# Kernel tuning notes

Measured on AMD Instinct MI355X. Metric: run time of the kernel, lower is better.

Reference implementation:

```python
import jax, jax.numpy as jnp
import numpy as np

B, S, R, C_Q, C_KV, H, C_A = 1, 128, 256, 256, 256, 8, 32


def setup_inputs() -> dict:
    key = jax.random.key(0)
    ks = jax.random.split(key, 11)
    scale = 0.02
    q = jax.random.normal(ks[0], (B, S, R, C_Q), jnp.float32)
    kv = jax.random.normal(ks[1], (B, S, R, C_KV), jnp.float32)
    bias = jax.random.normal(ks[2], (B, 1, R, R, H), jnp.float32)
    bias_mask = jax.random.randint(ks[3], (B, S, R), 0, 2).astype(jnp.float32)
    w_q = jax.random.normal(ks[4], (C_Q, H, C_A), jnp.float32) * scale
    w_k = jax.random.normal(ks[5], (C_KV, H, C_A), jnp.float32) * scale
    w_v = jax.random.normal(ks[6], (C_KV, H, C_A), jnp.float32) * scale
    w_g = jax.random.normal(ks[7], (C_Q, H, C_A), jnp.float32) * scale
    b_g = jax.random.normal(ks[8], (H, C_A), jnp.float32) * scale
    w_o = jax.random.normal(ks[9], (H, C_A, C_Q), jnp.float32) * scale
    b_o = jax.random.normal(ks[10], (C_Q,), jnp.float32) * scale
    return {"q": q, "kv": kv, "bias": bias, "bias_mask": bias_mask,
            "w_q": w_q, "w_k": w_k, "w_v": w_v, "w_g": w_g, "b_g": b_g,
            "w_o": w_o, "b_o": b_o}


def reference(q, kv, bias, bias_mask, w_q, w_k, w_v, w_g, b_g, w_o, b_o):
    # q, kv: [B, S, R, C]; attention over residue dim R within each row s.
    c_a = w_q.shape[-1]
    normsize = 1.0 / jnp.sqrt(jnp.asarray(c_a, q.dtype))
    Q = jnp.einsum('bsqc,chd->bsqhd', q, w_q) * normsize  # [B,S,R,H,Ca]
    K = jnp.einsum('bskc,chd->bskhd', kv, w_k)
    V = jnp.einsum('bskc,chd->bskhd', kv, w_v)
    # affinity: [B,S,Q,K,H]
    AT = jnp.einsum('bsqhd,bskhd->bsqkh', Q, K)
    mask_bias = (bias_mask[:, :, None, :, None] - 1.0) * 1e9  # [B,S,1,K,1]
    AT = AT + bias + mask_bias
    AT = jax.nn.softmax(AT, axis=-2)  # softmax over K
    O = jnp.einsum('bsqkh,bskhd->bsqhd', AT, V)
    G = jax.nn.sigmoid(jnp.einsum('bsqc,chd->bsqhd', q, w_g) + b_g)
    O = O * G
    out = jnp.einsum('bsqhd,hdc->bsqc', O, w_o) + b_o  # [B,S,R,C_Q]
    return out
```

## Files before the change

kernel.cpp:

```cpp
#include <hip/hip_runtime.h>

typedef __bf16 bf16;
typedef __bf16 bf16x8 __attribute__((ext_vector_type(8)));
typedef float  f32x4  __attribute__((ext_vector_type(4)));
typedef unsigned int u32;

#define MFMA16(a, b, c) __builtin_amdgcn_mfma_f32_16x16x32_bf16((a), (b), (c), 0, 0, 0)


typedef __attribute__((address_space(3))) u32 lds_u32;
typedef const __attribute__((address_space(1))) u32 glob_u32;
__device__ __forceinline__ void gll16(const void* g, void* l) {
    __builtin_amdgcn_global_load_lds((glob_u32*)g, (lds_u32*)l, 16, 0, 0);
}

__global__ __launch_bounds__(256) void prep_kernel(
    const float* __restrict__ q, const float* __restrict__ kv,
    const float* __restrict__ bias,
    const float* __restrict__ w_q, const float* __restrict__ w_k,
    const float* __restrict__ w_v, const float* __restrict__ w_g,
    const float* __restrict__ w_o,
    bf16* __restrict__ qbf, bf16* __restrict__ kvbf, float* __restrict__ biasT,
    bf16* __restrict__ Wqg, bf16* __restrict__ Wkv, bf16* __restrict__ Wo)
{
    const float norm = 0.17677669529663687f;
    const int gid = blockIdx.x * 256 + threadIdx.x;
    const int gsz = gridDim.x * 256;

    for (int u = gid; u < 2097152; u += gsz) {
        const float* src; bf16* dst;
        if (u < 1048576) { src = q + (size_t)u * 8;            dst = qbf  + (size_t)u * 8; }
        else             { src = kv + (size_t)(u - 1048576)*8; dst = kvbf + (size_t)(u - 1048576)*8; }
        float4 x0 = *(const float4*)(src);
        float4 x1 = *(const float4*)(src + 4);
        bf16x8 t;
        t[0]=(bf16)x0.x; t[1]=(bf16)x0.y; t[2]=(bf16)x0.z; t[3]=(bf16)x0.w;
        t[4]=(bf16)x1.x; t[5]=(bf16)x1.y; t[6]=(bf16)x1.z; t[7]=(bf16)x1.w;
        *(bf16x8*)dst = t;
    }
    for (int u = gid; u < 524288; u += gsz) {
        int h = u >> 16, qq = (u >> 8) & 255, kk = u & 255;
        biasT[u] = bias[(((qq << 8) + kk) << 3) + h];
    }
    for (int u = gid; u < 131072; u += gsz) {
        int n = u >> 8, k = u & 255;
        float v = (n < 256) ? w_q[k * 256 + n] * norm : w_g[k * 256 + (n - 256)];
        Wqg[u] = (bf16)v;
    }
    for (int u = gid; u < 131072; u += gsz) {
        int n = u >> 8, k = u & 255;
        float v = (n < 256) ? w_k[k * 256 + n] : w_v[k * 256 + (n - 256)];
        Wkv[u] = (bf16)v;
    }
    for (int u = gid; u < 65536; u += gsz) {
        int n = u >> 8, k = u & 255;
        Wo[u] = (bf16)w_o[k * 256 + n];
    }
}

template<bool F32OUT>
__device__ __forceinline__ void gemm_core(
    const bf16* __restrict__ A, const bf16* __restrict__ Bw,
    bf16* __restrict__ Cb, float* __restrict__ Cf, const float* __restrict__ bo,
    int m0, int n0, int ntot)
{
    __shared__ __align__(16) bf16 As[128 * 32];
    __shared__ __align__(16) bf16 Bs[128 * 32];

    const int tid  = threadIdx.x;
    const int lane = tid & 63, wave = tid >> 6;
    const int quad = lane >> 4, lc = lane & 15;
    const int wr = wave >> 1, wc = wave & 1;

    const int r0 = tid >> 2, p0 = tid & 3;
    const int c1 = tid + 256;
    const int r1 = (c1 & 255) >> 2, p1 = c1 & 3;
    const bf16* gA0 = A  + (size_t)(m0 + r0) * 256 + p0 * 8;
    const bf16* gA1 = A  + (size_t)(m0 + 64 + r0) * 256 + p0 * 8;
    const bf16* gB0 = Bw + (size_t)(n0 + r0) * 256 + p0 * 8;
    const bf16* gB1 = Bw + (size_t)(n0 + 64 + r0) * 256 + p0 * 8;
    bf16* lA0 = As + tid * 8;
    bf16* lA1 = As + (tid + 256) * 8;
    bf16* lB0 = Bs + tid * 8;
    bf16* lB1 = Bs + (tid + 256) * 8;
    (void)r1; (void)p1;

    f32x4 acc[4][4];
    #pragma unroll
    for (int i = 0; i < 4; ++i)
        #pragma unroll
        for (int j = 0; j < 4; ++j) acc[i][j] = f32x4{0.f, 0.f, 0.f, 0.f};

    #pragma unroll 1
    for (int kb = 0; kb < 8; ++kb) {
        const int ko = kb * 32;
        gll16(gA0 + ko, lA0);
        gll16(gA1 + ko, lA1);
        gll16(gB0 + ko, lB0);
        gll16(gB1 + ko, lB1);
        __syncthreads();

        bf16x8 aF[4], bF[4];
        #pragma unroll
        for (int mt = 0; mt < 4; ++mt)
            aF[mt] = *(const bf16x8*)(As + (wr * 64 + mt * 16 + lc) * 32 + quad * 8);
        #pragma unroll
        for (int nt = 0; nt < 4; ++nt)
            bF[nt] = *(const bf16x8*)(Bs + (wc * 64 + nt * 16 + lc) * 32 + quad * 8);
        #pragma unroll
        for (int mt = 0; mt < 4; ++mt)
            #pragma unroll
            for (int nt = 0; nt < 4; ++nt)
                acc[mt][nt] = MFMA16(aF[mt], bF[nt], acc[mt][nt]);
        __syncthreads();
    }

    #pragma unroll
    for (int mt = 0; mt < 4; ++mt) {
        #pragma unroll
        for (int nt = 0; nt < 4; ++nt) {
            const int row = m0 + wr * 64 + mt * 16 + quad * 4;
            const int col = n0 + wc * 64 + nt * 16 + lc;
            if (F32OUT) {
                float b = bo[col];
                #pragma unroll
                for (int rr = 0; rr < 4; ++rr)
                    Cf[(size_t)(row + rr) * ntot + col] = acc[mt][nt][rr] + b;
            } else {
                #pragma unroll
                for (int rr = 0; rr < 4; ++rr)
                    Cb[(size_t)(row + rr) * ntot + col] = (bf16)acc[mt][nt][rr];
            }
        }
    }
}


__global__ __launch_bounds__(256) void proj_kernel(
    const bf16* __restrict__ qbf, const bf16* __restrict__ kvbf,
    const bf16* __restrict__ Wqg, const bf16* __restrict__ Wkv,
    bf16* __restrict__ QG, bf16* __restrict__ KV)
{
    int bid = blockIdx.x;
    bool sel = bid >= 1024;
    int b = sel ? bid - 1024 : bid;
    int m0 = (b >> 2) * 128, n0 = (b & 3) * 128;
    gemm_core<false>(sel ? kvbf : qbf, sel ? Wkv : Wqg,
                     sel ? KV : QG, nullptr, nullptr, m0, n0, 512);
}

__global__ __launch_bounds__(256) void outproj_kernel(
    const bf16* __restrict__ OG, const bf16* __restrict__ Wo,
    const float* __restrict__ bo, float* __restrict__ out)
{
    int b = blockIdx.x;
    int m0 = (b >> 1) * 128, n0 = (b & 1) * 128;
    gemm_core<true>(OG, Wo, nullptr, out, bo, m0, n0, 256);
}

#define A_OFF_MASK 0
#define A_OFF_K    1024
#define A_OFF_VT   21504
#define A_OFF_P    38400
#define A_LDS_TOT  (38400 + 4 * 16 * 264 * 2)

__global__ __launch_bounds__(256) void attn_kernel(
    const bf16* __restrict__ QG, const bf16* __restrict__ KV,
    const float* __restrict__ biasT, const float* __restrict__ bias_mask,
    const float* __restrict__ b_g, bf16* __restrict__ OG)
{
    __shared__ __align__(16) char smem[A_LDS_TOT];
    float* maskadd = (float*)(smem + A_OFF_MASK);
    bf16*  Ks      = (bf16*)(smem + A_OFF_K);
    bf16*  Vt      = (bf16*)(smem + A_OFF_VT);

    const int tid  = threadIdx.x;
    const int wave = tid >> 6, lane = tid & 63;
    const int quad = lane >> 4, lc = lane & 15;
    const int h = blockIdx.x & 7;
    const int s = blockIdx.x >> 3;

    maskadd[tid] = (bias_mask[s * 256 + tid] - 1.0f) * 1e9f;
    {
        const bf16* kvrow = KV + (size_t)(s * 256 + tid) * 512 + h * 32;
        #pragma unroll
        for (int j = 0; j < 4; ++j)
            *(bf16x8*)(Ks + tid * 40 + j * 8) = *(const bf16x8*)(kvrow + j * 8);
        bf16x8 vx[4];
        #pragma unroll
        for (int j = 0; j < 4; ++j) vx[j] = *(const bf16x8*)(kvrow + 256 + j * 8);
        #pragma unroll
        for (int d = 0; d < 32; ++d)
            Vt[d * 264 + tid] = vx[d >> 3][d & 7];
    }
    __syncthreads();

    bf16* P = (bf16*)(smem + A_OFF_P) + wave * (16 * 264);
    const bf16* qgbase = QG + (size_t)(s * 256) * 512 + h * 32;

    #pragma unroll 1
    for (int p = 0; p < 4; ++p) {
        const int q0 = (wave * 4 + p) * 16;

        bf16x8 qf = *(const bf16x8*)(qgbase + (size_t)(q0 + lc) * 512 + quad * 8);

        f32x4 sc[16];
        #pragma unroll
        for (int kt = 0; kt < 16; ++kt) {
            bf16x8 kf = *(const bf16x8*)(Ks + (kt * 16 + lc) * 40 + quad * 8);
            f32x4 z = {0.f, 0.f, 0.f, 0.f};
            sc[kt] = MFMA16(qf, kf, z);
        }

        const float* bT = biasT + (((size_t)h * 256 + q0 + quad * 4) << 8);
        float sum[4] = {0.f, 0.f, 0.f, 0.f};
        #pragma unroll
        for (int kt = 0; kt < 16; ++kt) {
            float mv = maskadd[kt * 16 + lc];
            #pragma unroll
            for (int rr = 0; rr < 4; ++rr) {
                float e = __expf(sc[kt][rr] + bT[rr * 256 + kt * 16 + lc] + mv);
                sc[kt][rr] = e;
                sum[rr] += e;
            }
        }
        #pragma unroll
        for (int rr = 0; rr < 4; ++rr) {
            #pragma unroll
            for (int off = 8; off; off >>= 1) sum[rr] += __shfl_xor(sum[rr], off, 64);
        }
        float inv[4];
        #pragma unroll
        for (int rr = 0; rr < 4; ++rr) inv[rr] = 1.0f / sum[rr];

        #pragma unroll
        for (int kt = 0; kt < 16; ++kt)
            #pragma unroll
            for (int rr = 0; rr < 4; ++rr)
                P[(quad * 4 + rr) * 264 + kt * 16 + lc] = (bf16)(sc[kt][rr] * inv[rr]);

        f32x4 o0 = {0.f,0.f,0.f,0.f}, o1 = {0.f,0.f,0.f,0.f};
        #pragma unroll
        for (int ks = 0; ks < 8; ++ks) {
            bf16x8 pf = *(const bf16x8*)(P + lc * 264 + ks * 32 + quad * 8);
            bf16x8 v0 = *(const bf16x8*)(Vt + lc * 264 + ks * 32 + quad * 8);
            bf16x8 v1 = *(const bf16x8*)(Vt + (16 + lc) * 264 + ks * 32 + quad * 8);
            o0 = MFMA16(pf, v0, o0);
            o1 = MFMA16(pf, v1, o1);
        }

        const bf16* gbase = QG + (size_t)(s * 256) * 512 + 256 + h * 32;
        size_t obase = ((size_t)(s * 256 + q0 + quad * 4)) * 256 + h * 32;
        #pragma unroll
        for (int nt = 0; nt < 2; ++nt) {
            f32x4 ov = nt ? o1 : o0;
            float bg = b_g[h * 32 + nt * 16 + lc];
            #pragma unroll
            for (int rr = 0; rr < 4; ++rr) {
                float gp = (float)gbase[(size_t)(q0 + quad * 4 + rr) * 512 + nt * 16 + lc] + bg;
                float g = 1.0f / (1.0f + __expf(-gp));
                OG[obase + (size_t)rr * 256 + nt * 16 + lc] = (bf16)(ov[rr] * g);
            }
        }
    }
}

extern "C" void kernel_launch(void* const* d_in, const int* in_sizes, int n_in,
                              void* d_out, int out_size, void* d_ws, size_t ws_size,
                              hipStream_t stream)
{
    (void)in_sizes; (void)n_in; (void)out_size; (void)ws_size;
    const float* q    = (const float*)d_in[0];
    const float* kv   = (const float*)d_in[1];
    const float* bias = (const float*)d_in[2];
    const float* mask = (const float*)d_in[3];
    const float* w_q  = (const float*)d_in[4];
    const float* w_k  = (const float*)d_in[5];
    const float* w_v  = (const float*)d_in[6];
    const float* w_g  = (const float*)d_in[7];
    const float* b_g  = (const float*)d_in[8];
    const float* w_o  = (const float*)d_in[9];
    const float* b_o  = (const float*)d_in[10];
    float* out = (float*)d_out;

    char* ws = (char*)d_ws;
    bf16*  qbf   = (bf16*)(ws + 0);
    bf16*  kvbf  = (bf16*)(ws + 16777216);
    bf16*  QG    = (bf16*)(ws + 33554432);
    bf16*  KV    = (bf16*)(ws + 67108864);
    float* biasT = (float*)(ws + 100663296);
    bf16*  Wqg   = (bf16*)(ws + 102760448);
    bf16*  Wkv   = (bf16*)(ws + 103022592);
    bf16*  Wo    = (bf16*)(ws + 103284736);
    bf16*  OG    = qbf;

    prep_kernel<<<1024, 256, 0, stream>>>(q, kv, bias, w_q, w_k, w_v, w_g, w_o,
                                          qbf, kvbf, biasT, Wqg, Wkv, Wo);
    proj_kernel<<<2048, 256, 0, stream>>>(qbf, kvbf, Wqg, Wkv, QG, KV);
    attn_kernel<<<1024, 256, 0, stream>>>(QG, KV, biasT, mask, b_g, OG);
    outproj_kernel<<<512, 256, 0, stream>>>(OG, Wo, b_o, out);
}
```

Before: 235.0 us.

## Keep softmax probabilities in registers via permlane swaps, transpose MFMA operands

Attention now computes the transposed score tile so each lane holds one query row. The probabilities are packed to bf16 and rearranged across lanes with permlane32/permlane16 swaps to feed the PV MFMA directly, which removes the per-wave LDS P buffer and its store/load round trip. Normalization moves to the output stage, bias and mask loads become vectorized float4 reads, and gate loads and output stores are vectorized. LDS shrinks and launch bounds request 4 blocks per CU to raise occupancy. The GEMM block-index mapping also changes so consecutive blocks walk along M instead of N.

```diff
diff --git a/kernel.cpp b/kernel.cpp
--- a/kernel.cpp
+++ b/kernel.cpp
@@ -2,8 +2,12 @@
 
 typedef __bf16 bf16;
 typedef __bf16 bf16x8 __attribute__((ext_vector_type(8)));
+typedef __bf16 bf16x4 __attribute__((ext_vector_type(4)));
 typedef float  f32x4  __attribute__((ext_vector_type(4)));
 typedef unsigned int u32;
+typedef unsigned int u32x2 __attribute__((ext_vector_type(2)));
+typedef unsigned int u32x4 __attribute__((ext_vector_type(4)));
+typedef unsigned short u16;
 
 #define MFMA16(a, b, c) __builtin_amdgcn_mfma_f32_16x16x32_bf16((a), (b), (c), 0, 0, 0)
 
@@ -12,6 +16,12 @@
 typedef const __attribute__((address_space(1))) u32 glob_u32;
 __device__ __forceinline__ void gll16(const void* g, void* l) {
     __builtin_amdgcn_global_load_lds((glob_u32*)g, (lds_u32*)l, 16, 0, 0);
+}
+
+__device__ __forceinline__ u32 pk2(float lo, float hi) {
+    u16 a = __builtin_bit_cast(u16, (bf16)lo);
+    u16 b = __builtin_bit_cast(u16, (bf16)hi);
+    return ((u32)b << 16) | (u32)a;
 }
 
 __global__ __launch_bounds__(256) void prep_kernel(
@@ -73,8 +83,6 @@
     const int wr = wave >> 1, wc = wave & 1;
 
     const int r0 = tid >> 2, p0 = tid & 3;
-    const int c1 = tid + 256;
-    const int r1 = (c1 & 255) >> 2, p1 = c1 & 3;
     const bf16* gA0 = A  + (size_t)(m0 + r0) * 256 + p0 * 8;
     const bf16* gA1 = A  + (size_t)(m0 + 64 + r0) * 256 + p0 * 8;
     const bf16* gB0 = Bw + (size_t)(n0 + r0) * 256 + p0 * 8;
@@ -83,7 +91,6 @@
     bf16* lA1 = As + (tid + 256) * 8;
     bf16* lB0 = Bs + tid * 8;
     bf16* lB1 = Bs + (tid + 256) * 8;
-    (void)r1; (void)p1;
 
     f32x4 acc[4][4];
     #pragma unroll
@@ -135,7 +142,6 @@
     }
 }
 
-
 __global__ __launch_bounds__(256) void proj_kernel(
     const bf16* __restrict__ qbf, const bf16* __restrict__ kvbf,
     const bf16* __restrict__ Wqg, const bf16* __restrict__ Wkv,
@@ -144,7 +150,7 @@
     int bid = blockIdx.x;
     bool sel = bid >= 1024;
     int b = sel ? bid - 1024 : bid;
-    int m0 = (b >> 2) * 128, n0 = (b & 3) * 128;
+    int m0 = (b & 255) * 128, n0 = (b >> 8) * 128;
     gemm_core<false>(sel ? kvbf : qbf, sel ? Wkv : Wqg,
                      sel ? KV : QG, nullptr, nullptr, m0, n0, 512);
 }
@@ -154,17 +160,16 @@
     const float* __restrict__ bo, float* __restrict__ out)
 {
     int b = blockIdx.x;
-    int m0 = (b >> 1) * 128, n0 = (b & 1) * 128;
+    int m0 = (b & 255) * 128, n0 = (b >> 8) * 128;
     gemm_core<true>(OG, Wo, nullptr, out, bo, m0, n0, 256);
 }
 
 #define A_OFF_MASK 0
 #define A_OFF_K    1024
 #define A_OFF_VT   21504
-#define A_OFF_P    38400
-#define A_LDS_TOT  (38400 + 4 * 16 * 264 * 2)
-
-__global__ __launch_bounds__(256) void attn_kernel(
+#define A_LDS_TOT  (21504 + 32 * 264 * 2)
+
+__global__ __launch_bounds__(256, 4) void attn_kernel(
     const bf16* __restrict__ QG, const bf16* __restrict__ KV,
     const float* __restrict__ biasT, const float* __restrict__ bias_mask,
     const float* __restrict__ b_g, bf16* __restrict__ OG)
@@ -195,72 +200,73 @@
     }
     __syncthreads();
 
-    bf16* P = (bf16*)(smem + A_OFF_P) + wave * (16 * 264);
-    const bf16* qgbase = QG + (size_t)(s * 256) * 512 + h * 32;
+    const f32x4 bg0 = *(const f32x4*)(b_g + h * 32 + quad * 4);
+    const f32x4 bg1 = *(const f32x4*)(b_g + h * 32 + 16 + quad * 4);
 
     #pragma unroll 1
     for (int p = 0; p < 4; ++p) {
         const int q0 = (wave * 4 + p) * 16;
 
-        bf16x8 qf = *(const bf16x8*)(qgbase + (size_t)(q0 + lc) * 512 + quad * 8);
+        bf16x8 qf = *(const bf16x8*)(QG + (size_t)(s * 256 + q0 + lc) * 512 + h * 32 + quad * 8);
 
         f32x4 sc[16];
         #pragma unroll
         for (int kt = 0; kt < 16; ++kt) {
             bf16x8 kf = *(const bf16x8*)(Ks + (kt * 16 + lc) * 40 + quad * 8);
             f32x4 z = {0.f, 0.f, 0.f, 0.f};
-            sc[kt] = MFMA16(qf, kf, z);
-        }
-
-        const float* bT = biasT + (((size_t)h * 256 + q0 + quad * 4) << 8);
-        float sum[4] = {0.f, 0.f, 0.f, 0.f};
+            sc[kt] = MFMA16(kf, qf, z);
+        }
+
+        const float* bT = biasT + (((size_t)h * 256 + q0 + lc) << 8) + quad * 4;
+        float sum = 0.f;
         #pragma unroll
         for (int kt = 0; kt < 16; ++kt) {
-            float mv = maskadd[kt * 16 + lc];
+            f32x4 bv = *(const f32x4*)(bT + kt * 16);
+            f32x4 mv = *(const f32x4*)(maskadd + kt * 16 + quad * 4);
             #pragma unroll
             for (int rr = 0; rr < 4; ++rr) {
-                float e = __expf(sc[kt][rr] + bT[rr * 256 + kt * 16 + lc] + mv);
+                float e = __expf(sc[kt][rr] + bv[rr] + mv[rr]);
                 sc[kt][rr] = e;
-                sum[rr] += e;
+                sum += e;
             }
         }
-        #pragma unroll
-        for (int rr = 0; rr < 4; ++rr) {
-            #pragma unroll
-            for (int off = 8; off; off >>= 1) sum[rr] += __shfl_xor(sum[rr], off, 64);
-        }
-        float inv[4];
-        #pragma unroll
-        for (int rr = 0; rr < 4; ++rr) inv[rr] = 1.0f / sum[rr];
-
-        #pragma unroll
-        for (int kt = 0; kt < 16; ++kt)
-            #pragma unroll
-            for (int rr = 0; rr < 4; ++rr)
-                P[(quad * 4 + rr) * 264 + kt * 16 + lc] = (bf16)(sc[kt][rr] * inv[rr]);
-
-        f32x4 o0 = {0.f,0.f,0.f,0.f}, o1 = {0.f,0.f,0.f,0.f};
+        sum += __shfl_xor(sum, 16, 64);
+        sum += __shfl_xor(sum, 32, 64);
+        const float inv = 1.0f / sum;
+
+        f32x4 o0 = {0.f, 0.f, 0.f, 0.f}, o1 = {0.f, 0.f, 0.f, 0.f};
         #pragma unroll
         for (int ks = 0; ks < 8; ++ks) {
-            bf16x8 pf = *(const bf16x8*)(P + lc * 264 + ks * 32 + quad * 8);
+            u32 c0 = pk2(sc[2 * ks][0],     sc[2 * ks][1]);
+            u32 c1 = pk2(sc[2 * ks][2],     sc[2 * ks][3]);
+            u32 c2 = pk2(sc[2 * ks + 1][0], sc[2 * ks + 1][1]);
+            u32 c3 = pk2(sc[2 * ks + 1][2], sc[2 * ks + 1][3]);
+            u32x2 s02 = __builtin_amdgcn_permlane32_swap(c0, c2, false, false);
+            u32x2 s13 = __builtin_amdgcn_permlane32_swap(c1, c3, false, false);
+            u32x2 e02 = __builtin_amdgcn_permlane16_swap(s02.x, s02.y, false, false);
+            u32x2 e13 = __builtin_amdgcn_permlane16_swap(s13.x, s13.y, false, false);
+            u32x4 pw = {e02.x, e13.x, e02.y, e13.y};
+            bf16x8 pf = __builtin_bit_cast(bf16x8, pw);
             bf16x8 v0 = *(const bf16x8*)(Vt + lc * 264 + ks * 32 + quad * 8);
             bf16x8 v1 = *(const bf16x8*)(Vt + (16 + lc) * 264 + ks * 32 + quad * 8);
-            o0 = MFMA16(pf, v0, o0);
-            o1 = MFMA16(pf, v1, o1);
-        }
-
-        const bf16* gbase = QG + (size_t)(s * 256) * 512 + 256 + h * 32;
-        size_t obase = ((size_t)(s * 256 + q0 + quad * 4)) * 256 + h * 32;
+            o0 = MFMA16(v0, pf, o0);
+            o1 = MFMA16(v1, pf, o1);
+        }
+
+        const bf16* gp = QG + (size_t)(s * 256 + q0 + lc) * 512 + 256 + h * 32 + quad * 4;
+        bf16*       op = OG + (size_t)(s * 256 + q0 + lc) * 256 + h * 32 + quad * 4;
         #pragma unroll
         for (int nt = 0; nt < 2; ++nt) {
             f32x4 ov = nt ? o1 : o0;
-            float bg = b_g[h * 32 + nt * 16 + lc];
+            f32x4 bg = nt ? bg1 : bg0;
+            bf16x4 gv = *(const bf16x4*)(gp + nt * 16);
+            bf16x4 ob;
             #pragma unroll
             for (int rr = 0; rr < 4; ++rr) {
-                float gp = (float)gbase[(size_t)(q0 + quad * 4 + rr) * 512 + nt * 16 + lc] + bg;
-                float g = 1.0f / (1.0f + __expf(-gp));
-                OG[obase + (size_t)rr * 256 + nt * 16 + lc] = (bf16)(ov[rr] * g);
+                float g = 1.0f / (1.0f + __expf(-((float)gv[rr] + bg[rr])));
+                ob[rr] = (bf16)(ov[rr] * inv * g);
             }
+            *(bf16x4*)(op + nt * 16) = ob;
         }
     }
 }
```

New measurement: 351.3 us. 1.5x slower.
